# Performance work log

Measured on AMD Instinct MI355X. Metric: run time of the kernel, lower is better.

The kernel has to match this reference:

```python
import jax, jax.numpy as jnp
import numpy as np

DIM = 4096
N_HEADS = 32
HEAD_DIM = 128
N_KV_HEADS = 8
KV_REPEATS = N_HEADS // N_KV_HEADS
SLIDING_WINDOW = 4096
SEQLEN = 2048
ROPE_THETA = 10000.0


def calculate_rope(x, cos_freq, sin_freq):
    # x: (S, H, D); cos/sin: (S, D//2). Rotates interleaved pairs (Mistral RoPE).
    S, H, D = x.shape
    xr = x.reshape(S, H, D // 2, 2)
    x1, x2 = xr[..., 0], xr[..., 1]
    c = cos_freq[:, None, :]
    s = sin_freq[:, None, :]
    o1 = x1 * c - x2 * s
    o2 = x1 * s + x2 * c
    return jnp.stack([o1, o2], axis=-1).reshape(S, H, D)


def setup_inputs() -> dict:
    key = jax.random.key(0)
    k0, k1, k2 = jax.random.split(key, 3)
    x = jax.random.normal(k0, (SEQLEN, DIM), dtype=jnp.float32)
    positions = jnp.arange(SEQLEN, dtype=jnp.int32)
    # RoPE frequencies
    inv_freq = 1.0 / (ROPE_THETA ** (np.arange(0, HEAD_DIM, 2, dtype=np.float32) / HEAD_DIM))
    angles = np.arange(SEQLEN, dtype=np.float32)[:, None] * inv_freq[None, :]
    cos_freq = jnp.asarray(np.cos(angles), dtype=jnp.float32)
    sin_freq = jnp.asarray(np.sin(angles), dtype=jnp.float32)
    # additive causal + sliding-window mask: 0 where allowed, -1e9 where masked
    i = np.arange(SEQLEN)
    allowed = (i[None, :] <= i[:, None]) & ((i[:, None] - i[None, :]) < SLIDING_WINDOW)
    mask = jnp.asarray(np.where(allowed, 0.0, -1e9), dtype=jnp.float32)
    cache_k = jnp.zeros((SLIDING_WINDOW, N_KV_HEADS, HEAD_DIM), dtype=jnp.float32)
    cache_v = jnp.zeros((SLIDING_WINDOW, N_KV_HEADS, HEAD_DIM), dtype=jnp.float32)
    total_head_dim = (N_HEADS + 2 * N_KV_HEADS) * HEAD_DIM
    Wqkv = jax.random.normal(k1, (total_head_dim, DIM), dtype=jnp.float32) * 0.02
    Wo = jax.random.normal(k2, (DIM, N_HEADS * HEAD_DIM), dtype=jnp.float32) * 0.02
    return {"x": x, "cos_freq": cos_freq, "sin_freq": sin_freq, "positions": positions,
            "mask": mask, "cache_k": cache_k, "cache_v": cache_v, "Wqkv": Wqkv, "Wo": Wo}


def reference(x, cos_freq, sin_freq, positions, mask, cache_k, cache_v, Wqkv, Wo):
    # Prefill branch (positions.shape[0] > 1) of Attention.__call__
    seqlen = x.shape[0]
    scale = HEAD_DIM ** (-0.5)
    s1 = N_HEADS * HEAD_DIM
    s2 = s1 + N_KV_HEADS * HEAD_DIM
    xqkv = x @ Wqkv.T                                  # (S, 6144)
    xq, xk, xv = jnp.split(xqkv, [s1, s2], axis=-1)
    xq = xq.reshape(seqlen, N_HEADS, HEAD_DIM)
    xk = xk.reshape(seqlen, N_KV_HEADS, HEAD_DIM)
    xv = xv.reshape(seqlen, N_KV_HEADS, HEAD_DIM)
    xq = calculate_rope(xq, cos_freq, sin_freq)
    xk = calculate_rope(xk, cos_freq, sin_freq)
    # KV-cache update (scatter; positions all in range here)
    cache_k = cache_k.at[positions, :, :].set(xk[positions, :, :], mode="drop")
    cache_v = cache_v.at[positions, :, :].set(xv[positions, :, :], mode="drop")
    # GQA repeat: (S, n_kv, D) -> (S, n_heads, D)
    k = jnp.repeat(xk, KV_REPEATS, axis=1)
    v = jnp.repeat(xv, KV_REPEATS, axis=1)
    q = jnp.transpose(xq, (1, 0, 2))                   # (H, S, D)
    k = jnp.transpose(k, (1, 0, 2))
    v = jnp.transpose(v, (1, 0, 2))
    scores = jnp.einsum("hqd,hkd->hqk", q, k) * scale  # (H, S, S)
    scores = scores + mask[jnp.newaxis, ...]
    probs = jax.nn.softmax(scores.astype(jnp.float32), axis=-1).astype(q.dtype)
    out = jnp.einsum("hqk,hkd->hqd", probs, v)         # (H, S, D)
    out = jnp.transpose(out, (1, 0, 2)).reshape(seqlen, -1)
    output = out @ Wo.T                                # (S, dim)
    return (output, cache_k, cache_v)
```

## Files before the change

### kernel.cpp

```cpp
#include <hip/hip_runtime.h>
#include <stdint.h>

typedef __bf16   bf16x8 __attribute__((ext_vector_type(8)));
typedef float    f32x4  __attribute__((ext_vector_type(4)));
typedef uint16_t u16x8  __attribute__((ext_vector_type(8)));

__device__ __forceinline__ uint16_t f2bf(float f) {
  uint32_t b = __builtin_bit_cast(uint32_t, f);
  b += 0x7fffu + ((b >> 16) & 1u);
  return (uint16_t)(b >> 16);
}
__device__ __forceinline__ float bf2f(uint16_t u) {
  return __builtin_bit_cast(float, ((uint32_t)u) << 16);
}
__device__ __forceinline__ u16x8 ldcvt8(const float* __restrict__ p) {
  f32x4 lo = *(const f32x4*)p;
  f32x4 hi = *(const f32x4*)(p + 4);
  u16x8 o;
  o[0] = f2bf(lo[0]); o[1] = f2bf(lo[1]); o[2] = f2bf(lo[2]); o[3] = f2bf(lo[3]);
  o[4] = f2bf(hi[0]); o[5] = f2bf(hi[1]); o[6] = f2bf(hi[2]); o[7] = f2bf(hi[3]);
  return o;
}

typedef const __attribute__((address_space(1))) uint32_t cga_u32;
typedef __attribute__((address_space(3))) uint32_t lds_u32;
__device__ __forceinline__ void gload16(const uint16_t* g, uint16_t* l) {
  __builtin_amdgcn_global_load_lds((cga_u32*)g, (lds_u32*)l, 16, 0, 0);
}

__global__ __launch_bounds__(256) void cast_kernel(const float* __restrict__ in,
                                                   uint16_t* __restrict__ out, int n8) {
  int i = blockIdx.x * 256 + threadIdx.x;
  if (i >= n8) return;
  u16x8 o = ldcvt8(in + (size_t)i * 8);
  *(u16x8*)(out + (size_t)i * 8) = o;
}

__global__ __launch_bounds__(256) void copy2_kernel(const float* __restrict__ a, float* __restrict__ da,
                                                    const float* __restrict__ b, float* __restrict__ db,
                                                    int n4) {
  int i = blockIdx.x * 256 + threadIdx.x;
  if (i >= n4) return;
  *(f32x4*)(da + (size_t)i * 4) = *(const f32x4*)(a + (size_t)i * 4);
  *(f32x4*)(db + (size_t)i * 4) = *(const f32x4*)(b + (size_t)i * 4);
}

template <int OUT_BF16>
__global__ __launch_bounds__(512, 2) void gemm256(const uint16_t* __restrict__ A,
                                                  const uint16_t* __restrict__ B,
                                                  void* __restrict__ Cout,
                                                  int M, int N, int K) {
  __shared__ __align__(16) uint16_t AS[3][256 * 64];
  __shared__ __align__(16) uint16_t BS[2][256 * 64];
  const int tid = threadIdx.x;
  const int lane = tid & 63, wave = tid >> 6;
  const int l16 = lane & 15, quad = lane >> 4;
  const int wm = wave >> 2;
  const int wn = wave & 3;
  const int bm = blockIdx.y, bn = blockIdx.x;
  const int NT = K >> 6;

  f32x4 acc[8][4] = {};

  const int sr = tid >> 3;
  const int sc = ((tid & 7) ^ (sr & 7)) << 3;
  const uint16_t* Asrc = A + (size_t)(bm * 256 + sr) * K + sc;
  const uint16_t* Bsrc = B + (size_t)(bn * 256 + sr) * K + sc;
  const size_t rs64 = (size_t)64 * K;

  int aoff[8][2], boff[4][2];
#pragma unroll
  for (int mr = 0; mr < 8; mr++)
#pragma unroll
    for (int ks = 0; ks < 2; ks++)
      aoff[mr][ks] = (wm * 128 + mr * 16 + l16) * 128 +
                     (((ks << 6) | (quad << 4)) ^ ((l16 & 7) << 4));
#pragma unroll
  for (int nr = 0; nr < 4; nr++)
#pragma unroll
    for (int ks = 0; ks < 2; ks++)
      boff[nr][ks] = (wn * 64 + nr * 16 + l16) * 128 +
                     (((ks << 6) | (quad << 4)) ^ ((l16 & 7) << 4));

  auto stageA = [&](int buf, int h, int t) {
    const uint16_t* s = Asrc + (size_t)(h * 128) * K + (size_t)t * 64;
    uint16_t* d = &AS[buf][h * 8192 + tid * 8];
    gload16(s, d);
    gload16(s + rs64, d + 4096);
  };
  auto stageB = [&](int buf, int h, int t) {
    const uint16_t* s = Bsrc + (size_t)(h * 128) * K + (size_t)t * 64;
    uint16_t* d = &BS[buf][h * 8192 + tid * 8];
    gload16(s, d);
    gload16(s + rs64, d + 4096);
  };

  stageA(0, 0, 0); stageA(0, 1, 0); stageB(0, 0, 0); stageB(0, 1, 0);
  stageA(1, 0, 1); stageA(1, 1, 1);
  asm volatile("s_waitcnt vmcnt(4)" ::: "memory");
  __builtin_amdgcn_s_barrier();

  int ca = 0;
  for (int t = 0; t < NT; t++) {
    const int cb = t & 1, nb = cb ^ 1;
    const int na3 = (ca + 2 >= 3) ? ca - 1 : ca + 2;
    const char* Ab = (const char*)AS[ca];
    const char* Bb = (const char*)BS[cb];
    bf16x8 aF[4][2], bF[4][2];

#pragma unroll
    for (int m4 = 0; m4 < 4; m4++)
#pragma unroll
      for (int ks = 0; ks < 2; ks++)
        aF[m4][ks] = __builtin_bit_cast(bf16x8, *(const u16x8*)(Ab + aoff[m4][ks]));
#pragma unroll
    for (int n2 = 0; n2 < 2; n2++)
#pragma unroll
      for (int ks = 0; ks < 2; ks++)
        bF[n2][ks] = __builtin_bit_cast(bf16x8, *(const u16x8*)(Bb + boff[n2][ks]));
    if (t + 1 < NT) stageB(nb, 0, t + 1);
    __builtin_amdgcn_s_barrier();
    asm volatile("s_waitcnt lgkmcnt(0)" ::: "memory");
    __builtin_amdgcn_sched_barrier(0);
    __builtin_amdgcn_s_setprio(1);
#pragma unroll
    for (int m4 = 0; m4 < 4; m4++)
#pragma unroll
      for (int n2 = 0; n2 < 2; n2++)
#pragma unroll
        for (int ks = 0; ks < 2; ks++)
          acc[m4][n2] = __builtin_amdgcn_mfma_f32_16x16x32_bf16(aF[m4][ks], bF[n2][ks], acc[m4][n2], 0, 0, 0);
    __builtin_amdgcn_s_setprio(0);
    __builtin_amdgcn_s_barrier();

#pragma unroll
    for (int n2 = 0; n2 < 2; n2++)
#pragma unroll
      for (int ks = 0; ks < 2; ks++)
        bF[2 + n2][ks] = __builtin_bit_cast(bf16x8, *(const u16x8*)(Bb + boff[2 + n2][ks]));
    if (t + 1 < NT) stageB(nb, 1, t + 1);
    __builtin_amdgcn_s_barrier();
    asm volatile("s_waitcnt lgkmcnt(0)" ::: "memory");
    __builtin_amdgcn_sched_barrier(0);
    __builtin_amdgcn_s_setprio(1);
#pragma unroll
    for (int m4 = 0; m4 < 4; m4++)
#pragma unroll
      for (int n2 = 0; n2 < 2; n2++)
#pragma unroll
        for (int ks = 0; ks < 2; ks++)
          acc[m4][2 + n2] = __builtin_amdgcn_mfma_f32_16x16x32_bf16(aF[m4][ks], bF[2 + n2][ks], acc[m4][2 + n2], 0, 0, 0);
    __builtin_amdgcn_s_setprio(0);
    __builtin_amdgcn_s_barrier();

#pragma unroll
    for (int m4 = 0; m4 < 4; m4++)
#pragma unroll
      for (int ks = 0; ks < 2; ks++)
        aF[m4][ks] = __builtin_bit_cast(bf16x8, *(const u16x8*)(Ab + aoff[4 + m4][ks]));
    if (t + 2 < NT) stageA(na3, 0, t + 2);
    __builtin_amdgcn_s_barrier();
    asm volatile("s_waitcnt lgkmcnt(0)" ::: "memory");
    __builtin_amdgcn_sched_barrier(0);
    __builtin_amdgcn_s_setprio(1);
#pragma unroll
    for (int m4 = 0; m4 < 4; m4++)
#pragma unroll
      for (int n2 = 0; n2 < 2; n2++)
#pragma unroll
        for (int ks = 0; ks < 2; ks++)
          acc[4 + m4][n2] = __builtin_amdgcn_mfma_f32_16x16x32_bf16(aF[m4][ks], bF[n2][ks], acc[4 + m4][n2], 0, 0, 0);
    __builtin_amdgcn_s_setprio(0);
    __builtin_amdgcn_s_barrier();

    if (t + 2 < NT) stageA(na3, 1, t + 2);
    if (t < NT - 2) asm volatile("s_waitcnt vmcnt(4)" ::: "memory");
    else            asm volatile("s_waitcnt vmcnt(0)" ::: "memory");
    __builtin_amdgcn_s_barrier();
    __builtin_amdgcn_s_setprio(1);
#pragma unroll
    for (int m4 = 0; m4 < 4; m4++)
#pragma unroll
      for (int n2 = 0; n2 < 2; n2++)
#pragma unroll
        for (int ks = 0; ks < 2; ks++)
          acc[4 + m4][2 + n2] = __builtin_amdgcn_mfma_f32_16x16x32_bf16(aF[m4][ks], bF[2 + n2][ks], acc[4 + m4][2 + n2], 0, 0, 0);
    __builtin_amdgcn_s_setprio(0);
    __builtin_amdgcn_s_barrier();

    ca = (ca == 2) ? 0 : ca + 1;
  }

  const int row0 = bm * 256 + wm * 128 + quad * 4;
  const int col0 = bn * 256 + wn * 64 + l16;
#pragma unroll
  for (int mr = 0; mr < 8; mr++)
#pragma unroll
    for (int nr = 0; nr < 4; nr++)
#pragma unroll
      for (int r = 0; r < 4; r++) {
        size_t idx = (size_t)(row0 + mr * 16 + r) * N + (col0 + nr * 16);
        if constexpr (OUT_BF16) ((uint16_t*)Cout)[idx] = f2bf(acc[mr][nr][r]);
        else                    ((float*)Cout)[idx]    = acc[mr][nr][r];
      }
}

template <int OUT_BF16>
__global__ __launch_bounds__(256) void gemm_nt_bf16(const uint16_t* __restrict__ A,
                                                    const uint16_t* __restrict__ B,
                                                    void* __restrict__ Cout,
                                                    int M, int N, int K) {
  __shared__ __align__(16) uint16_t As[128 * 32];
  __shared__ __align__(16) uint16_t Bs[128 * 32];
  const int tid = threadIdx.x;
  const int lane = tid & 63, wave = tid >> 6;
  const int l16 = lane & 15, quad = lane >> 4;
  const int wm = (wave & 1) << 6, wn = (wave >> 1) << 6;
  const int bm = blockIdx.y, bn = blockIdx.x;

  f32x4 acc[4][4] = {};

  const int srow = wave * 16 + (lane >> 2);
  const int schunk = lane & 3;
  const uint16_t* Ag = A + (size_t)(bm * 128 + srow) * K + schunk * 8;
  const uint16_t* Bg = B + (size_t)(bn * 128 + srow) * K + schunk * 8;
  const size_t rs64 = (size_t)64 * K;
  uint16_t* AsD0 = &As[srow * 32 + schunk * 8];
  uint16_t* AsD1 = AsD0 + 64 * 32;
  uint16_t* BsD0 = &Bs[srow * 32 + schunk * 8];
  uint16_t* BsD1 = BsD0 + 64 * 32;

  for (int k0 = 0; k0 < K; k0 += 32) {
    gload16(Ag, AsD0);
    gload16(Ag + rs64, AsD1);
    gload16(Bg, BsD0);
    gload16(Bg + rs64, BsD1);
    Ag += 32; Bg += 32;
    __syncthreads();
    bf16x8 af[4], bfr[4];
#pragma unroll
    for (int i = 0; i < 4; i++) {
      af[i]  = __builtin_bit_cast(bf16x8, *(const u16x8*)&As[(wm + i * 16 + l16) * 32 + quad * 8]);
      bfr[i] = __builtin_bit_cast(bf16x8, *(const u16x8*)&Bs[(wn + i * 16 + l16) * 32 + quad * 8]);
    }
#pragma unroll
    for (int i = 0; i < 4; i++)
#pragma unroll
      for (int j = 0; j < 4; j++)
        acc[i][j] = __builtin_amdgcn_mfma_f32_16x16x32_bf16(af[i], bfr[j], acc[i][j], 0, 0, 0);
    __syncthreads();
  }

  const int row0 = bm * 128 + wm + quad * 4;
  const int col0 = bn * 128 + wn + l16;
#pragma unroll
  for (int i = 0; i < 4; i++)
#pragma unroll
    for (int j = 0; j < 4; j++)
#pragma unroll
      for (int r = 0; r < 4; r++) {
        size_t idx = (size_t)(row0 + i * 16 + r) * N + (col0 + j * 16);
        if constexpr (OUT_BF16) ((uint16_t*)Cout)[idx] = f2bf(acc[i][j][r]);
        else                    ((float*)Cout)[idx]    = acc[i][j][r];
      }
}

template <int A_BF16, int OUT_BF16>
__global__ __launch_bounds__(256) void gemm_bt(const void* __restrict__ Ap,
                                               const float* __restrict__ B,
                                               void* __restrict__ Cout, int M, int N, int K) {
  constexpr int PAD = 40;
  __shared__ __align__(16) uint16_t As[128 * PAD];
  __shared__ __align__(16) uint16_t Bs[128 * PAD];
  const int tid = threadIdx.x;
  const int lane = tid & 63, wave = tid >> 6;
  const int l16 = lane & 15, quad = lane >> 4;
  const int wm = (wave & 1) << 6, wn = (wave >> 1) << 6;
  const int bm = blockIdx.y, bn = blockIdx.x;

  f32x4 acc[4][4] = {};

  const int srow = tid >> 2;
  const int scol = (tid & 3) << 3;
  const size_t aoff = (size_t)(bm * 128 + srow) * K + scol;
  const uint16_t* Agh = (const uint16_t*)Ap + aoff;
  const float*    Agf = (const float*)Ap + aoff;
  const float*    Bg  = B + (size_t)(bn * 128 + srow) * K + scol;
  const size_t rstride = (size_t)64 * K;

  for (int k0 = 0; k0 < K; k0 += 32) {
    u16x8 a0, a1;
    if constexpr (A_BF16) {
      a0 = *(const u16x8*)Agh;
      a1 = *(const u16x8*)(Agh + rstride);
      Agh += 32;
    } else {
      a0 = ldcvt8(Agf);
      a1 = ldcvt8(Agf + rstride);
      Agf += 32;
    }
    u16x8 b0 = ldcvt8(Bg);
    u16x8 b1 = ldcvt8(Bg + rstride);
    Bg += 32;
    __syncthreads();
    *(u16x8*)&As[srow * PAD + scol] = a0;
    *(u16x8*)&As[(srow + 64) * PAD + scol] = a1;
    *(u16x8*)&Bs[srow * PAD + scol] = b0;
    *(u16x8*)&Bs[(srow + 64) * PAD + scol] = b1;
    __syncthreads();
    bf16x8 af[4], bfr[4];
#pragma unroll
    for (int i = 0; i < 4; i++) {
      af[i]  = __builtin_bit_cast(bf16x8, *(const u16x8*)&As[(wm + i * 16 + l16) * PAD + quad * 8]);
      bfr[i] = __builtin_bit_cast(bf16x8, *(const u16x8*)&Bs[(wn + i * 16 + l16) * PAD + quad * 8]);
    }
#pragma unroll
    for (int i = 0; i < 4; i++)
#pragma unroll
      for (int j = 0; j < 4; j++)
        acc[i][j] = __builtin_amdgcn_mfma_f32_16x16x32_bf16(af[i], bfr[j], acc[i][j], 0, 0, 0);
  }

  const int row0 = bm * 128 + wm + quad * 4;
  const int col0 = bn * 128 + wn + l16;
#pragma unroll
  for (int i = 0; i < 4; i++)
#pragma unroll
    for (int j = 0; j < 4; j++)
#pragma unroll
      for (int r = 0; r < 4; r++) {
        size_t idx = (size_t)(row0 + i * 16 + r) * N + (col0 + j * 16);
        if constexpr (OUT_BF16) ((uint16_t*)Cout)[idx] = f2bf(acc[i][j][r]);
        else                    ((float*)Cout)[idx]    = acc[i][j][r];
      }
}

__global__ __launch_bounds__(256) void rope_kernel(const uint16_t* __restrict__ xqkv,
    const float* __restrict__ cosf, const float* __restrict__ sinf,
    const int* __restrict__ pos,
    uint16_t* __restrict__ qb, uint16_t* __restrict__ kb, uint16_t* __restrict__ vb,
    float* __restrict__ ck, float* __restrict__ cv) {
  const float QS = 0.12751743f;
  const int s = blockIdx.x;
  const int e0 = (blockIdx.y * 256 + threadIdx.x) * 8;
  const int head = e0 >> 7;
  const int d0 = e0 & 127;
  u16x8 u = *(const u16x8*)(xqkv + (size_t)s * 6144 + e0);
  float x[8];
#pragma unroll
  for (int j = 0; j < 8; j++) x[j] = bf2f(u[j]);

  if (head < 40) {
    const int i0 = d0 >> 1;
    f32x4 c4 = *(const f32x4*)(cosf + (size_t)s * 64 + i0);
    f32x4 s4 = *(const f32x4*)(sinf + (size_t)s * 64 + i0);
    float o[8];
#pragma unroll
    for (int kk = 0; kk < 4; kk++) {
      float x1 = x[2 * kk], x2 = x[2 * kk + 1];
      o[2 * kk]     = x1 * c4[kk] - x2 * s4[kk];
      o[2 * kk + 1] = x1 * s4[kk] + x2 * c4[kk];
    }
    if (head < 32) {
      u16x8 ob;
#pragma unroll
      for (int j = 0; j < 8; j++) ob[j] = f2bf(o[j] * QS);
      *(u16x8*)(qb + (size_t)s * 4096 + head * 128 + d0) = ob;
    } else {
      u16x8 ob;
#pragma unroll
      for (int j = 0; j < 8; j++) ob[j] = f2bf(o[j]);
      int kvh = head - 32;
      *(u16x8*)(kb + ((size_t)kvh * 2048 + s) * 128 + d0) = ob;
      int p = pos[s];
      if ((unsigned)p < 4096u) {
        float* dst = ck + ((size_t)p * 8 + kvh) * 128 + d0;
#pragma unroll
        for (int j = 0; j < 8; j++) dst[j] = o[j];
      }
    }
  } else {
    int kvh = head - 40;
    *(u16x8*)(vb + ((size_t)kvh * 2048 + s) * 128 + d0) = u;
    int p = pos[s];
    if ((unsigned)p < 4096u) {
      float* dst = cv + ((size_t)p * 8 + kvh) * 128 + d0;
#pragma unroll
      for (int j = 0; j < 8; j++) dst[j] = x[j];
    }
  }
}

__global__ __launch_bounds__(256) void vtrans_kernel(const uint16_t* __restrict__ vb,
                                                     uint16_t* __restrict__ vt) {
  __shared__ __align__(16) uint16_t t[32 * 72];
  const int h = blockIdx.z;
  const int s0 = blockIdx.x * 64, d0 = blockIdx.y * 32;
  const uint16_t* in = vb + (size_t)h * 2048 * 128;
  uint16_t* out = vt + (size_t)h * 128 * 2048;
  const int tid = threadIdx.x;
  {
    int r = tid >> 2, c8 = (tid & 3) * 8;
    u16x8 v = *(const u16x8*)(in + (size_t)(s0 + r) * 128 + d0 + c8);
#pragma unroll
    for (int j = 0; j < 8; j++) t[(c8 + j) * 72 + r] = v[j];
  }
  __syncthreads();
  {
    int r = tid >> 3, c8 = (tid & 7) * 8;
    u16x8 v = *(const u16x8*)&t[r * 72 + c8];
    *(u16x8*)(out + (size_t)(d0 + r) * 2048 + s0 + c8) = v;
  }
}

__global__ __launch_bounds__(256) void flash_kernel(const uint16_t* __restrict__ Qb,
    const uint16_t* __restrict__ Kb, const uint16_t* __restrict__ Vtb,
    uint16_t* __restrict__ Ob) {
  __shared__ __align__(16) uint16_t Ks[64 * 128];
  __shared__ __align__(16) uint16_t Vts[128 * 64];
  __shared__ __align__(16) uint16_t Ps[4][16 * 64];
  const int tid = threadIdx.x;
  const int lane = tid & 63, wave = tid >> 6;
  const int l16 = lane & 15, quad = lane >> 4;
  const int h = blockIdx.y, kvh = h >> 2;
  const uint16_t* Kg = Kb + (size_t)kvh * 2048 * 128;
  const uint16_t* Vg = Vtb + (size_t)kvh * 128 * 2048;

  u16x8 kreg[4], vreg[4];
  const int krr = tid >> 4, kcb = (tid & 15) * 16;
  const int vrr = tid >> 3, vcb = (tid & 7) * 16;

  for (int ph = 0; ph < 2; ph++) {
    const int qtile = ph ? (int)blockIdx.x : 31 - (int)blockIdx.x;
    const int qb = qtile * 64;
    const int nch = qtile + 1;
    const int qmax = qb + wave * 16 + 15;

    bf16x8 qf[4];
    {
      const uint16_t* Qg = Qb + (size_t)(qb + wave * 16 + l16) * 4096 + h * 128 + quad * 8;
#pragma unroll
      for (int dc = 0; dc < 4; dc++)
        qf[dc] = __builtin_bit_cast(bf16x8, *(const u16x8*)(Qg + dc * 32));
    }

    f32x4 oacc[8] = {};
    float m_run[4], l_run[4];
#pragma unroll
    for (int r = 0; r < 4; r++) { m_run[r] = -1e30f; l_run[r] = 0.f; }

#pragma unroll
    for (int i = 0; i < 4; i++)
      kreg[i] = *(const u16x8*)(Kg + (size_t)(krr + i * 16) * 128 + kcb / 2);
#pragma unroll
    for (int i = 0; i < 4; i++)
      vreg[i] = *(const u16x8*)(Vg + (size_t)(vrr + i * 32) * 2048 + vcb / 2);

    for (int ch = 0; ch < nch; ch++) {
      const int cb = ch * 64;
#pragma unroll
      for (int i = 0; i < 4; i++) {
        int r = krr + i * 16;
        *(u16x8*)((char*)Ks + r * 256 + (kcb ^ ((r & 7) << 4))) = kreg[i];
      }
#pragma unroll
      for (int i = 0; i < 4; i++) {
        int r = vrr + i * 32;
        *(u16x8*)((char*)Vts + r * 128 + (vcb ^ ((r & 7) << 4))) = vreg[i];
      }
      __syncthreads();

      if (ch + 1 < nch) {
        const int nb = cb + 64;
#pragma unroll
        for (int i = 0; i < 4; i++)
          kreg[i] = *(const u16x8*)(Kg + (size_t)(nb + krr + i * 16) * 128 + kcb / 2);
#pragma unroll
        for (int i = 0; i < 4; i++)
          vreg[i] = *(const u16x8*)(Vg + (size_t)(vrr + i * 32) * 2048 + nb + vcb / 2);
      }

      f32x4 sacc[4] = {};
      __builtin_amdgcn_s_setprio(1);
#pragma unroll
      for (int ni = 0; ni < 4; ni++) {
        if (cb + ni * 16 <= qmax) {
#pragma unroll
          for (int dc = 0; dc < 4; dc++) {
            int r = ni * 16 + l16;
            bf16x8 kf = __builtin_bit_cast(bf16x8,
                *(const u16x8*)((const char*)Ks + r * 256 + ((dc * 64 + quad * 16) ^ ((r & 7) << 4))));
            sacc[ni] = __builtin_amdgcn_mfma_f32_16x16x32_bf16(qf[dc], kf, sacc[ni], 0, 0, 0);
          }
        }
      }
      __builtin_amdgcn_s_setprio(0);

      float p[4][4], alpha[4];
#pragma unroll
      for (int reg = 0; reg < 4; reg++) {
        const int q = qb + wave * 16 + quad * 4 + reg;
        float mx = -1e30f;
#pragma unroll
        for (int ni = 0; ni < 4; ni++) {
          float sv = sacc[ni][reg];
          if (cb + ni * 16 + l16 > q) sv = -1e30f;
          p[ni][reg] = sv;
          mx = fmaxf(mx, sv);
        }
#pragma unroll
        for (int off = 8; off >= 1; off >>= 1)
          mx = fmaxf(mx, __shfl_xor(mx, off, 64));
        float mn = fmaxf(m_run[reg], mx);
        alpha[reg] = __builtin_amdgcn_exp2f(m_run[reg] - mn);
        m_run[reg] = mn;
        float rs = 0.f;
#pragma unroll
        for (int ni = 0; ni < 4; ni++) {
          float e = __builtin_amdgcn_exp2f(p[ni][reg] - mn);
          p[ni][reg] = e;
          rs += e;
        }
#pragma unroll
        for (int off = 8; off >= 1; off >>= 1)
          rs += __shfl_xor(rs, off, 64);
        l_run[reg] = l_run[reg] * alpha[reg] + rs;
      }

#pragma unroll
      for (int dt = 0; dt < 8; dt++)
#pragma unroll
        for (int reg = 0; reg < 4; reg++)
          oacc[dt][reg] *= alpha[reg];

      uint16_t* Pw = Ps[wave];
#pragma unroll
      for (int ni = 0; ni < 4; ni++)
#pragma unroll
        for (int reg = 0; reg < 4; reg++) {
          int r = quad * 4 + reg;
          *(uint16_t*)((char*)Pw + r * 128 + ((ni * 32 + l16 * 2) ^ ((r & 7) << 4))) =
              f2bf(p[ni][reg]);
        }

      __builtin_amdgcn_s_setprio(1);
#pragma unroll
      for (int kc = 0; kc < 2; kc++) {
        if (cb + kc * 32 <= qmax) {
          bf16x8 pf = __builtin_bit_cast(bf16x8,
              *(const u16x8*)((const char*)Pw + l16 * 128 + ((kc * 64 + quad * 16) ^ ((l16 & 7) << 4))));
#pragma unroll
          for (int dt = 0; dt < 8; dt++) {
            int r = dt * 16 + l16;
            bf16x8 vf = __builtin_bit_cast(bf16x8,
                *(const u16x8*)((const char*)Vts + r * 128 + ((kc * 64 + quad * 16) ^ ((r & 7) << 4))));
            oacc[dt] = __builtin_amdgcn_mfma_f32_16x16x32_bf16(pf, vf, oacc[dt], 0, 0, 0);
          }
        }
      }
      __builtin_amdgcn_s_setprio(0);

      __syncthreads();
    }

#pragma unroll
    for (int dt = 0; dt < 8; dt++)
#pragma unroll
      for (int reg = 0; reg < 4; reg++) {
        float o = oacc[dt][reg] / l_run[reg];
        int row = qb + wave * 16 + quad * 4 + reg;
        int col = h * 128 + dt * 16 + l16;
        Ob[(size_t)row * 4096 + col] = f2bf(o);
      }
  }
}

extern "C" void kernel_launch(void* const* d_in, const int* in_sizes, int n_in,
                              void* d_out, int out_size, void* d_ws, size_t ws_size,
                              hipStream_t stream) {
  const float* x     = (const float*)d_in[0];
  const float* cosf  = (const float*)d_in[1];
  const float* sinf  = (const float*)d_in[2];
  const int*   pos   = (const int*)d_in[3];
  const float* ck_in = (const float*)d_in[5];
  const float* cv_in = (const float*)d_in[6];
  const float* Wqkv  = (const float*)d_in[7];
  const float* Wo    = (const float*)d_in[8];

  float* out    = (float*)d_out;
  float* ck_out = out + (size_t)2048 * 4096;
  float* cv_out = ck_out + (size_t)4096 * 8 * 128;

  char* ws = (char*)d_ws;

  if (ws_size >= 104857600ull) {
    uint16_t* xqkv_bf = (uint16_t*)(ws);
    uint16_t* attn_bf = (uint16_t*)(ws);
    uint16_t* x_bf    = (uint16_t*)(ws + 25165824);
    uint16_t* q_bf    = (uint16_t*)(ws + 25165824);
    uint16_t* k_bf    = (uint16_t*)(ws + 41943040);
    uint16_t* v_bf    = (uint16_t*)(ws + 46137344);
    uint16_t* vt_bf   = (uint16_t*)(ws + 50331648);
    uint16_t* wq_bf   = (uint16_t*)(ws + 54525952);
    uint16_t* wo_bf   = (uint16_t*)(ws + 54525952);

    cast_kernel<<<4096, 256, 0, stream>>>(x, x_bf, 1048576);
    cast_kernel<<<12288, 256, 0, stream>>>(Wqkv, wq_bf, 3145728);

    bool ok256 = true;
    gemm256<1><<<dim3(24, 8), 512, 0, stream>>>(x_bf, wq_bf, xqkv_bf, 2048, 6144, 4096);
    if (hipGetLastError() != hipSuccess) {
      ok256 = false;
      gemm_nt_bf16<1><<<dim3(48, 16), 256, 0, stream>>>(x_bf, wq_bf, xqkv_bf, 2048, 6144, 4096);
    }

    copy2_kernel<<<4096, 256, 0, stream>>>(ck_in, ck_out, cv_in, cv_out, 1048576);

    rope_kernel<<<dim3(2048, 3), 256, 0, stream>>>(xqkv_bf, cosf, sinf, pos,
                                                   q_bf, k_bf, v_bf, ck_out, cv_out);

    vtrans_kernel<<<dim3(32, 4, 8), 256, 0, stream>>>(v_bf, vt_bf);

    flash_kernel<<<dim3(16, 32), 256, 0, stream>>>(q_bf, k_bf, vt_bf, attn_bf);

    cast_kernel<<<8192, 256, 0, stream>>>(Wo, wo_bf, 2097152);

    if (ok256) {
      gemm256<0><<<dim3(16, 8), 512, 0, stream>>>(attn_bf, wo_bf, out, 2048, 4096, 4096);
      if (hipGetLastError() != hipSuccess)
        gemm_nt_bf16<0><<<dim3(32, 16), 256, 0, stream>>>(attn_bf, wo_bf, out, 2048, 4096, 4096);
    } else {
      gemm_nt_bf16<0><<<dim3(32, 16), 256, 0, stream>>>(attn_bf, wo_bf, out, 2048, 4096, 4096);
    }
  } else {
    uint16_t* xqkv_bf = (uint16_t*)(ws);
    uint16_t* attn_bf = (uint16_t*)(ws);
    uint16_t* q_bf    = (uint16_t*)(ws + 25165824);
    uint16_t* k_bf    = (uint16_t*)(ws + 41943040);
    uint16_t* v_bf    = (uint16_t*)(ws + 46137344);
    uint16_t* vt_bf   = (uint16_t*)(ws + 50331648);

    gemm_bt<0, 1><<<dim3(48, 16), 256, 0, stream>>>(x, Wqkv, xqkv_bf, 2048, 6144, 4096);
    copy2_kernel<<<4096, 256, 0, stream>>>(ck_in, ck_out, cv_in, cv_out, 1048576);
    rope_kernel<<<dim3(2048, 3), 256, 0, stream>>>(xqkv_bf, cosf, sinf, pos,
                                                   q_bf, k_bf, v_bf, ck_out, cv_out);
    vtrans_kernel<<<dim3(32, 4, 8), 256, 0, stream>>>(v_bf, vt_bf);
    flash_kernel<<<dim3(16, 32), 256, 0, stream>>>(q_bf, k_bf, vt_bf, attn_bf);
    gemm_bt<1, 0><<<dim3(32, 16), 256, 0, stream>>>(attn_bf, Wo, out, 2048, 4096, 4096);
  }
}
```

Baseline: 606.1 us.

## Add split-K to output GEMM and restructure gemm256 LDS double buffering

The 256x256 GEMM kernel gets a K-split parameter, and the output projection now runs as two K halves, doubling the grid from 128 to 256 blocks so more of the CUs are busy. The halves are written as fp32 partials and summed by a new add kernel. The LDS staging is reorganised into per-half A and B double buffers with full-tile prefetch two steps ahead. This reordering also changes the MFMA schedule of the QKV GEMM. The split costs an extra 64MB of partial-sum traffic plus one more launch, and relies on a larger workspace.

```diff
diff --git a/kernel.cpp b/kernel.cpp
--- a/kernel.cpp
+++ b/kernel.cpp
@@ -28,6 +28,8 @@
   __builtin_amdgcn_global_load_lds((cga_u32*)g, (lds_u32*)l, 16, 0, 0);
 }
 
+#define CBAR() do { asm volatile("" ::: "memory"); __builtin_amdgcn_s_barrier(); asm volatile("" ::: "memory"); } while (0)
+
 __global__ __launch_bounds__(256) void cast_kernel(const float* __restrict__ in,
                                                    uint16_t* __restrict__ out, int n8) {
   int i = blockIdx.x * 256 + threadIdx.x;
@@ -45,164 +47,172 @@
   *(f32x4*)(db + (size_t)i * 4) = *(const f32x4*)(b + (size_t)i * 4);
 }
 
+__global__ __launch_bounds__(256) void add2_kernel(const float* __restrict__ a,
+                                                   const float* __restrict__ b,
+                                                   float* __restrict__ o, int n4) {
+  int i = blockIdx.x * 256 + threadIdx.x;
+  if (i >= n4) return;
+  f32x4 x = *(const f32x4*)(a + (size_t)i * 4);
+  f32x4 y = *(const f32x4*)(b + (size_t)i * 4);
+  x[0] += y[0]; x[1] += y[1]; x[2] += y[2]; x[3] += y[3];
+  *(f32x4*)(o + (size_t)i * 4) = x;
+}
+
 template <int OUT_BF16>
 __global__ __launch_bounds__(512, 2) void gemm256(const uint16_t* __restrict__ A,
                                                   const uint16_t* __restrict__ B,
                                                   void* __restrict__ Cout,
-                                                  int M, int N, int K) {
-  __shared__ __align__(16) uint16_t AS[3][256 * 64];
-  __shared__ __align__(16) uint16_t BS[2][256 * 64];
+                                                  int M, int N, int K, int Klen) {
+  __shared__ __align__(16) uint16_t AS[2][2][128 * 64];
+  __shared__ __align__(16) uint16_t BS[2][2][128 * 64];
   const int tid = threadIdx.x;
   const int lane = tid & 63, wave = tid >> 6;
   const int l16 = lane & 15, quad = lane >> 4;
   const int wm = wave >> 2;
   const int wn = wave & 3;
   const int bm = blockIdx.y, bn = blockIdx.x;
-  const int NT = K >> 6;
+  const int Kbase = (int)blockIdx.z * Klen;
+  const int NT = Klen >> 6;
 
   f32x4 acc[8][4] = {};
 
   const int sr = tid >> 3;
   const int sc = ((tid & 7) ^ (sr & 7)) << 3;
-  const uint16_t* Asrc = A + (size_t)(bm * 256 + sr) * K + sc;
-  const uint16_t* Bsrc = B + (size_t)(bn * 256 + sr) * K + sc;
+  const uint16_t* Asrc = A + (size_t)(bm * 256 + sr) * K + Kbase + sc;
+  const uint16_t* Bsrc = B + (size_t)(bn * 256 + sr) * K + Kbase + sc;
   const size_t rs64 = (size_t)64 * K;
-
-  int aoff[8][2], boff[4][2];
+  const int dstoff = (tid >> 3) * 64 + (tid & 7) * 8;
+
+  int aoffB[8][2], boffB[4][2];
 #pragma unroll
   for (int mr = 0; mr < 8; mr++)
 #pragma unroll
-    for (int ks = 0; ks < 2; ks++)
-      aoff[mr][ks] = (wm * 128 + mr * 16 + l16) * 128 +
-                     (((ks << 6) | (quad << 4)) ^ ((l16 & 7) << 4));
+    for (int ks = 0; ks < 2; ks++) {
+      int la = mr * 16 + l16;
+      aoffB[mr][ks] = la * 128 + (((ks << 6) | (quad << 4)) ^ ((la & 7) << 4));
+    }
 #pragma unroll
   for (int nr = 0; nr < 4; nr++)
 #pragma unroll
-    for (int ks = 0; ks < 2; ks++)
-      boff[nr][ks] = (wn * 64 + nr * 16 + l16) * 128 +
-                     (((ks << 6) | (quad << 4)) ^ ((l16 & 7) << 4));
-
-  auto stageA = [&](int buf, int h, int t) {
+    for (int ks = 0; ks < 2; ks++) {
+      int lb = (wn & 1) * 64 + nr * 16 + l16;
+      boffB[nr][ks] = lb * 128 + (((ks << 6) | (quad << 4)) ^ ((lb & 7) << 4));
+    }
+
+  auto stageA = [&](int h, int p, int t) {
     const uint16_t* s = Asrc + (size_t)(h * 128) * K + (size_t)t * 64;
-    uint16_t* d = &AS[buf][h * 8192 + tid * 8];
+    uint16_t* d = &AS[h][p][dstoff];
     gload16(s, d);
     gload16(s + rs64, d + 4096);
   };
-  auto stageB = [&](int buf, int h, int t) {
+  auto stageB = [&](int h, int p, int t) {
     const uint16_t* s = Bsrc + (size_t)(h * 128) * K + (size_t)t * 64;
-    uint16_t* d = &BS[buf][h * 8192 + tid * 8];
+    uint16_t* d = &BS[h][p][dstoff];
     gload16(s, d);
     gload16(s + rs64, d + 4096);
   };
 
-  stageA(0, 0, 0); stageA(0, 1, 0); stageB(0, 0, 0); stageB(0, 1, 0);
-  stageA(1, 0, 1); stageA(1, 1, 1);
-  asm volatile("s_waitcnt vmcnt(4)" ::: "memory");
-  __builtin_amdgcn_s_barrier();
-
-  int ca = 0;
+  stageA(0, 0, 0); stageA(1, 0, 0); stageB(0, 0, 0); stageB(1, 0, 0);
+  if (1 < NT) { stageA(0, 1, 1); stageA(1, 1, 1); stageB(0, 1, 1); stageB(1, 1, 1);
+                asm volatile("s_waitcnt vmcnt(8)" ::: "memory"); }
+  else        { asm volatile("s_waitcnt vmcnt(0)" ::: "memory"); }
+  CBAR();
+
   for (int t = 0; t < NT; t++) {
-    const int cb = t & 1, nb = cb ^ 1;
-    const int na3 = (ca + 2 >= 3) ? ca - 1 : ca + 2;
-    const char* Ab = (const char*)AS[ca];
-    const char* Bb = (const char*)BS[cb];
-    bf16x8 aF[4][2], bF[4][2];
-
-#pragma unroll
-    for (int m4 = 0; m4 < 4; m4++)
+    const int p = t & 1;
+    const char* Ab = (const char*)AS[wm][p];
+    const char* Bb = (const char*)BS[wn >> 1][p];
+    bf16x8 aF0[4][2], aF4[4][2], bF[4][2];
+
+#pragma unroll
+    for (int m = 0; m < 4; m++)
 #pragma unroll
       for (int ks = 0; ks < 2; ks++)
-        aF[m4][ks] = __builtin_bit_cast(bf16x8, *(const u16x8*)(Ab + aoff[m4][ks]));
-#pragma unroll
-    for (int n2 = 0; n2 < 2; n2++)
-#pragma unroll
-      for (int ks = 0; ks < 2; ks++)
-        bF[n2][ks] = __builtin_bit_cast(bf16x8, *(const u16x8*)(Bb + boff[n2][ks]));
-    if (t + 1 < NT) stageB(nb, 0, t + 1);
-    __builtin_amdgcn_s_barrier();
+        aF0[m][ks] = __builtin_bit_cast(bf16x8, *(const u16x8*)(Ab + aoffB[m][ks]));
+#pragma unroll
+    for (int nr = 0; nr < 4; nr++)
+      bF[nr][0] = __builtin_bit_cast(bf16x8, *(const u16x8*)(Bb + boffB[nr][0]));
+    CBAR();
     asm volatile("s_waitcnt lgkmcnt(0)" ::: "memory");
     __builtin_amdgcn_sched_barrier(0);
     __builtin_amdgcn_s_setprio(1);
 #pragma unroll
-    for (int m4 = 0; m4 < 4; m4++)
-#pragma unroll
-      for (int n2 = 0; n2 < 2; n2++)
-#pragma unroll
-        for (int ks = 0; ks < 2; ks++)
-          acc[m4][n2] = __builtin_amdgcn_mfma_f32_16x16x32_bf16(aF[m4][ks], bF[n2][ks], acc[m4][n2], 0, 0, 0);
+    for (int m = 0; m < 4; m++)
+#pragma unroll
+      for (int nr = 0; nr < 4; nr++)
+        acc[m][nr] = __builtin_amdgcn_mfma_f32_16x16x32_bf16(aF0[m][0], bF[nr][0], acc[m][nr], 0, 0, 0);
     __builtin_amdgcn_s_setprio(0);
-    __builtin_amdgcn_s_barrier();
-
-#pragma unroll
-    for (int n2 = 0; n2 < 2; n2++)
+    CBAR();
+
+#pragma unroll
+    for (int m = 0; m < 4; m++)
 #pragma unroll
       for (int ks = 0; ks < 2; ks++)
-        bF[2 + n2][ks] = __builtin_bit_cast(bf16x8, *(const u16x8*)(Bb + boff[2 + n2][ks]));
-    if (t + 1 < NT) stageB(nb, 1, t + 1);
-    __builtin_amdgcn_s_barrier();
+        aF4[m][ks] = __builtin_bit_cast(bf16x8, *(const u16x8*)(Ab + aoffB[4 + m][ks]));
+#pragma unroll
+    for (int nr = 0; nr < 4; nr++)
+      bF[nr][1] = __builtin_bit_cast(bf16x8, *(const u16x8*)(Bb + boffB[nr][1]));
+    CBAR();
     asm volatile("s_waitcnt lgkmcnt(0)" ::: "memory");
     __builtin_amdgcn_sched_barrier(0);
     __builtin_amdgcn_s_setprio(1);
 #pragma unroll
-    for (int m4 = 0; m4 < 4; m4++)
-#pragma unroll
-      for (int n2 = 0; n2 < 2; n2++)
-#pragma unroll
-        for (int ks = 0; ks < 2; ks++)
-          acc[m4][2 + n2] = __builtin_amdgcn_mfma_f32_16x16x32_bf16(aF[m4][ks], bF[2 + n2][ks], acc[m4][2 + n2], 0, 0, 0);
+    for (int m = 0; m < 4; m++)
+#pragma unroll
+      for (int nr = 0; nr < 4; nr++)
+        acc[m][nr] = __builtin_amdgcn_mfma_f32_16x16x32_bf16(aF0[m][1], bF[nr][1], acc[m][nr], 0, 0, 0);
     __builtin_amdgcn_s_setprio(0);
-    __builtin_amdgcn_s_barrier();
-
-#pragma unroll
-    for (int m4 = 0; m4 < 4; m4++)
-#pragma unroll
-      for (int ks = 0; ks < 2; ks++)
-        aF[m4][ks] = __builtin_bit_cast(bf16x8, *(const u16x8*)(Ab + aoff[4 + m4][ks]));
-    if (t + 2 < NT) stageA(na3, 0, t + 2);
-    __builtin_amdgcn_s_barrier();
-    asm volatile("s_waitcnt lgkmcnt(0)" ::: "memory");
-    __builtin_amdgcn_sched_barrier(0);
+    CBAR();
+
+    if (t + 2 < NT) { stageA(0, p, t + 2); stageB(0, p, t + 2); }
+    CBAR();
     __builtin_amdgcn_s_setprio(1);
 #pragma unroll
-    for (int m4 = 0; m4 < 4; m4++)
-#pragma unroll
-      for (int n2 = 0; n2 < 2; n2++)
-#pragma unroll
-        for (int ks = 0; ks < 2; ks++)
-          acc[4 + m4][n2] = __builtin_amdgcn_mfma_f32_16x16x32_bf16(aF[m4][ks], bF[n2][ks], acc[4 + m4][n2], 0, 0, 0);
+    for (int m = 0; m < 4; m++)
+#pragma unroll
+      for (int nr = 0; nr < 4; nr++)
+        acc[4 + m][nr] = __builtin_amdgcn_mfma_f32_16x16x32_bf16(aF4[m][0], bF[nr][0], acc[4 + m][nr], 0, 0, 0);
     __builtin_amdgcn_s_setprio(0);
-    __builtin_amdgcn_s_barrier();
-
-    if (t + 2 < NT) stageA(na3, 1, t + 2);
-    if (t < NT - 2) asm volatile("s_waitcnt vmcnt(4)" ::: "memory");
-    else            asm volatile("s_waitcnt vmcnt(0)" ::: "memory");
-    __builtin_amdgcn_s_barrier();
+    CBAR();
+
+    if (t + 2 < NT) {
+      stageA(1, p, t + 2); stageB(1, p, t + 2);
+      asm volatile("s_waitcnt vmcnt(8)" ::: "memory");
+    } else {
+      asm volatile("s_waitcnt vmcnt(0)" ::: "memory");
+    }
+    CBAR();
     __builtin_amdgcn_s_setprio(1);
 #pragma unroll
-    for (int m4 = 0; m4 < 4; m4++)
-#pragma unroll
-      for (int n2 = 0; n2 < 2; n2++)
-#pragma unroll
-        for (int ks = 0; ks < 2; ks++)
-          acc[4 + m4][2 + n2] = __builtin_amdgcn_mfma_f32_16x16x32_bf16(aF[m4][ks], bF[2 + n2][ks], acc[4 + m4][2 + n2], 0, 0, 0);
+    for (int m = 0; m < 4; m++)
+#pragma unroll
+      for (int nr = 0; nr < 4; nr++)
+        acc[4 + m][nr] = __builtin_amdgcn_mfma_f32_16x16x32_bf16(aF4[m][1], bF[nr][1], acc[4 + m][nr], 0, 0, 0);
     __builtin_amdgcn_s_setprio(0);
-    __builtin_amdgcn_s_barrier();
-
-    ca = (ca == 2) ? 0 : ca + 1;
+    CBAR();
   }
 
   const int row0 = bm * 256 + wm * 128 + quad * 4;
   const int col0 = bn * 256 + wn * 64 + l16;
-#pragma unroll
-  for (int mr = 0; mr < 8; mr++)
-#pragma unroll
-    for (int nr = 0; nr < 4; nr++)
-#pragma unroll
-      for (int r = 0; r < 4; r++) {
-        size_t idx = (size_t)(row0 + mr * 16 + r) * N + (col0 + nr * 16);
-        if constexpr (OUT_BF16) ((uint16_t*)Cout)[idx] = f2bf(acc[mr][nr][r]);
-        else                    ((float*)Cout)[idx]    = acc[mr][nr][r];
-      }
+  if constexpr (OUT_BF16) {
+    uint16_t* C = (uint16_t*)Cout;
+#pragma unroll
+    for (int mr = 0; mr < 8; mr++)
+#pragma unroll
+      for (int nr = 0; nr < 4; nr++)
+#pragma unroll
+        for (int r = 0; r < 4; r++)
+          C[(size_t)(row0 + mr * 16 + r) * N + (col0 + nr * 16)] = f2bf(acc[mr][nr][r]);
+  } else {
+    float* C = (float*)Cout + (size_t)blockIdx.z * M * N;
+#pragma unroll
+    for (int mr = 0; mr < 8; mr++)
+#pragma unroll
+      for (int nr = 0; nr < 4; nr++)
+#pragma unroll
+        for (int r = 0; r < 4; r++)
+          C[(size_t)(row0 + mr * 16 + r) * N + (col0 + nr * 16)] = acc[mr][nr][r];
+  }
 }
 
 template <int OUT_BF16>
@@ -608,7 +618,7 @@
     cast_kernel<<<12288, 256, 0, stream>>>(Wqkv, wq_bf, 3145728);
 
     bool ok256 = true;
-    gemm256<1><<<dim3(24, 8), 512, 0, stream>>>(x_bf, wq_bf, xqkv_bf, 2048, 6144, 4096);
+    gemm256<1><<<dim3(24, 8, 1), 512, 0, stream>>>(x_bf, wq_bf, xqkv_bf, 2048, 6144, 4096, 4096);
     if (hipGetLastError() != hipSuccess) {
       ok256 = false;
       gemm_nt_bf16<1><<<dim3(48, 16), 256, 0, stream>>>(x_bf, wq_bf, xqkv_bf, 2048, 6144, 4096);
@@ -626,9 +636,20 @@
     cast_kernel<<<8192, 256, 0, stream>>>(Wo, wo_bf, 2097152);
 
     if (ok256) {
-      gemm256<0><<<dim3(16, 8), 512, 0, stream>>>(attn_bf, wo_bf, out, 2048, 4096, 4096);
-      if (hipGetLastError() != hipSuccess)
-        gemm_nt_bf16<0><<<dim3(32, 16), 256, 0, stream>>>(attn_bf, wo_bf, out, 2048, 4096, 4096);
+      if (ws_size >= 155189248ull) {
+        float* p0 = (float*)(ws + 88080384);
+        float* p1 = p0 + (size_t)2048 * 4096;
+        gemm256<0><<<dim3(16, 8, 2), 512, 0, stream>>>(attn_bf, wo_bf, p0, 2048, 4096, 4096, 2048);
+        if (hipGetLastError() == hipSuccess) {
+          add2_kernel<<<8192, 256, 0, stream>>>(p0, p1, out, 2097152);
+        } else {
+          gemm_nt_bf16<0><<<dim3(32, 16), 256, 0, stream>>>(attn_bf, wo_bf, out, 2048, 4096, 4096);
+        }
+      } else {
+        gemm256<0><<<dim3(16, 8, 1), 512, 0, stream>>>(attn_bf, wo_bf, out, 2048, 4096, 4096, 4096);
+        if (hipGetLastError() != hipSuccess)
+          gemm_nt_bf16<0><<<dim3(32, 16), 256, 0, stream>>>(attn_bf, wo_bf, out, 2048, 4096, 4096);
+      }
     } else {
       gemm_nt_bf16<0><<<dim3(32, 16), 256, 0, stream>>>(attn_bf, wo_bf, out, 2048, 4096, 4096);
     }
```

After: 591.6 us. 1.02x faster.
